# Performance work log

Measured on AMD Instinct MI355X. Metric: run time of the kernel, lower is better.

The kernel has to match this reference:

```python
import jax, jax.numpy as jnp
import numpy as np

NEG_SLOPE = 0.2


def _gat_layer(x, W, a_src, a_dst, b, src, dst, n_nodes):
    # x: [N, D_in], W: [D_in, D_out], a_src/a_dst: [D_out], b: [D_out]
    h = x @ W                                        # [N, D]
    e_src = h @ a_src                                # [N]
    e_dst = h @ a_dst                                # [N]
    e = jax.nn.leaky_relu(e_src[src] + e_dst[dst], NEG_SLOPE)  # [E]
    # segment softmax over incoming edges of each dst node
    m = jax.ops.segment_max(e, dst, num_segments=n_nodes)      # [N]
    w = jnp.exp(e - m[dst])                                    # [E]
    z = jax.ops.segment_sum(w, dst, num_segments=n_nodes)      # [N]
    alpha = w / z[dst]                                         # [E]
    out = jax.ops.segment_sum(h[src] * alpha[:, None], dst, num_segments=n_nodes)
    return out + b


def setup_inputs() -> dict:
    key = jax.random.key(0)
    ks = jax.random.split(key, 10)
    N, E, D = 10000, 100000, 768
    scale = 1.0 / np.sqrt(D)
    x = jax.random.normal(ks[0], (N, D), dtype=jnp.float32)
    edge_index = jax.random.randint(ks[1], (2, E), 0, N, dtype=jnp.int32)
    params = {}
    for i, nm in enumerate(["1", "2"]):
        params[f"W{nm}"] = jax.random.normal(ks[2 + 4 * i], (D, D), jnp.float32) * scale
        params[f"att_src{nm}"] = jax.random.normal(ks[3 + 4 * i], (D,), jnp.float32) * scale
        params[f"att_dst{nm}"] = jax.random.normal(ks[4 + 4 * i], (D,), jnp.float32) * scale
        params[f"b{nm}"] = jnp.zeros((D,), jnp.float32)
    return {"x": x, "edge_index": edge_index, **params}


def reference(x, edge_index, W1, att_src1, att_dst1, b1, W2, att_src2, att_dst2, b2):
    n_nodes = x.shape[0]
    loops = jnp.arange(n_nodes, dtype=edge_index.dtype)
    src = jnp.concatenate([edge_index[0], loops])  # add self loops (PyG default)
    dst = jnp.concatenate([edge_index[1], loops])
    h = _gat_layer(x, W1, att_src1, att_dst1, b1, src, dst, n_nodes)
    h = jax.nn.relu(h)
    out = _gat_layer(h, W2, att_src2, att_dst2, b2, src, dst, n_nodes)
    return out
```

## Files before the change

### kernel.cpp

```cpp
#include <hip/hip_runtime.h>
#include <hip/hip_bf16.h>

#define D_FEAT 768

typedef __bf16 bf16x8 __attribute__((ext_vector_type(8)));
typedef float floatx4 __attribute__((ext_vector_type(4)));

__device__ __forceinline__ float bf2f(unsigned short u) {
    unsigned int x = ((unsigned int)u) << 16;
    return __builtin_bit_cast(float, x);
}
__device__ __forceinline__ unsigned short f2bf(float f) {
    unsigned int x = __builtin_bit_cast(unsigned int, f);
    unsigned int lsb = (x >> 16) & 1u;
    x += 0x7fffu + lsb;
    return (unsigned short)(x >> 16);
}
__device__ __forceinline__ void async_ld16(const void* g, void* l) {
    __builtin_amdgcn_global_load_lds(
        (__attribute__((address_space(1))) void*)(g),
        (__attribute__((address_space(3))) void*)(l), 16, 0, 0);
}

__global__ __launch_bounds__(256) void conv_init_kernel(
    const float* __restrict__ x, unsigned short* __restrict__ xb, int n4,
    int* __restrict__ deg, float* __restrict__ es1, float* __restrict__ ed1,
    float* __restrict__ es2, float* __restrict__ ed2, int N)
{
    int i = blockIdx.x * 256 + threadIdx.x;
    if (i < n4) {
        float4 v = ((const float4*)x)[i];
        ushort4 o;
        o.x = f2bf(v.x); o.y = f2bf(v.y); o.z = f2bf(v.z); o.w = f2bf(v.w);
        ((ushort4*)xb)[i] = o;
    }
    if (i < N) {
        deg[i] = 1;
        es1[i] = 0.f; ed1[i] = 0.f; es2[i] = 0.f; ed2[i] = 0.f;
    }
}

__global__ __launch_bounds__(256) void transpose_kernel(
    const float* __restrict__ W1, const float* __restrict__ W2,
    unsigned short* __restrict__ Wt1, unsigned short* __restrict__ Wt2)
{
    const float* W = blockIdx.z ? W2 : W1;
    unsigned short* Wt = blockIdx.z ? Wt2 : Wt1;
    __shared__ float tile[32][33];
    int x0 = blockIdx.x * 32, y0 = blockIdx.y * 32;
    int tx = threadIdx.x & 31, ty = threadIdx.x >> 5;
    for (int r = ty; r < 32; r += 8)
        tile[r][tx] = W[(size_t)(y0 + r) * D_FEAT + x0 + tx];
    __syncthreads();
    for (int r = ty; r < 32; r += 8)
        Wt[(size_t)(x0 + r) * D_FEAT + y0 + tx] = f2bf(tile[tx][r]);
}

__global__ __launch_bounds__(256) void gemm_kernel(
    const unsigned short* __restrict__ A,
    const unsigned short* __restrict__ Bt,
    unsigned short* __restrict__ C,
    const float* __restrict__ vsrc, const float* __restrict__ vdst,
    float* __restrict__ es, float* __restrict__ ed, int M)
{
    __shared__ __align__(16) unsigned short sA[128 * 32];
    __shared__ __align__(16) unsigned short sB[128 * 32];

    const int tid = threadIdx.x;
    const int lane = tid & 63, wave = tid >> 6;
    const int m0 = blockIdx.x * 128, n0 = blockIdx.y * 128;
    const int wm = wave >> 1, wn = wave & 1;
    const int l15 = lane & 15, quad = lane >> 4;

    const int srow = lane >> 2;
    const int scol = (lane & 3) * 8;
    int ar0 = m0 + wave * 32 + srow;      if (ar0 >= M) ar0 = M - 1;
    int ar1 = m0 + wave * 32 + 16 + srow; if (ar1 >= M) ar1 = M - 1;
    const unsigned short* aptr0 = A + (size_t)ar0 * 768 + scol;
    const unsigned short* aptr1 = A + (size_t)ar1 * 768 + scol;
    const unsigned short* bptr0 = Bt + (size_t)(n0 + wave * 32 + srow) * 768 + scol;
    const unsigned short* bptr1 = bptr0 + (size_t)16 * 768;
    char* aldst = (char*)sA + wave * 2048;
    char* bldst = (char*)sB + wave * 2048;

    floatx4 acc[4][4];
    #pragma unroll
    for (int i = 0; i < 4; ++i)
        #pragma unroll
        for (int j = 0; j < 4; ++j)
            acc[i][j] = (floatx4){0.f, 0.f, 0.f, 0.f};

    for (int kt = 0; kt < 768; kt += 32) {
        __syncthreads();
        async_ld16(aptr0 + kt, aldst);
        async_ld16(aptr1 + kt, aldst + 1024);
        async_ld16(bptr0 + kt, bldst);
        async_ld16(bptr1 + kt, bldst + 1024);
        __syncthreads();

        bf16x8 af[4], bfr[4];
        #pragma unroll
        for (int i = 0; i < 4; ++i)
            af[i] = *(const bf16x8*)&sA[(wm * 64 + i * 16 + l15) * 32 + quad * 8];
        #pragma unroll
        for (int j = 0; j < 4; ++j)
            bfr[j] = *(const bf16x8*)&sB[(wn * 64 + j * 16 + l15) * 32 + quad * 8];
        #pragma unroll
        for (int i = 0; i < 4; ++i)
            #pragma unroll
            for (int j = 0; j < 4; ++j)
                acc[i][j] = __builtin_amdgcn_mfma_f32_16x16x32_bf16(af[i], bfr[j], acc[i][j], 0, 0, 0);
    }

    float as_[4], ad_[4];
    #pragma unroll
    for (int j = 0; j < 4; ++j) {
        int nn = n0 + wn * 64 + j * 16 + l15;
        as_[j] = vsrc[nn]; ad_[j] = vdst[nn];
    }

    #pragma unroll
    for (int i = 0; i < 4; ++i)
        #pragma unroll
        for (int r = 0; r < 4; ++r) {
            int m = m0 + wm * 64 + i * 16 + quad * 4 + r;
            float ps = 0.f, pd = 0.f;
            #pragma unroll
            for (int j = 0; j < 4; ++j) {
                float v = acc[i][j][r];
                ps += v * as_[j]; pd += v * ad_[j];
            }
            if (m < M) {
                #pragma unroll
                for (int j = 0; j < 4; ++j)
                    C[(size_t)m * 768 + n0 + wn * 64 + j * 16 + l15] = f2bf(acc[i][j][r]);
            }
            #pragma unroll
            for (int sh = 8; sh >= 1; sh >>= 1) {
                ps += __shfl_xor(ps, sh, 64);
                pd += __shfl_xor(pd, sh, 64);
            }
            if (l15 == 0 && m < M) {
                atomicAdd(&es[m], ps);
                atomicAdd(&ed[m], pd);
            }
        }
}

__global__ void count_kernel(const int* __restrict__ dst, int* __restrict__ deg, int e) {
    int i = blockIdx.x * blockDim.x + threadIdx.x;
    if (i < e) atomicAdd(&deg[dst[i]], 1);
}
__global__ __launch_bounds__(1024) void scan_kernel(
    const int* __restrict__ deg, int* __restrict__ row_ptr,
    int* __restrict__ cursor, int n)
{
    __shared__ int part[1024];
    int t = threadIdx.x;
    int per = (n + 1023) / 1024;
    int base = t * per;
    int s = 0;
    for (int i = 0; i < per; ++i) { int idx = base + i; if (idx < n) s += deg[idx]; }
    part[t] = s; __syncthreads();
    for (int off = 1; off < 1024; off <<= 1) {
        int v = (t >= off) ? part[t - off] : 0;
        __syncthreads();
        part[t] += v;
        __syncthreads();
    }
    int run = (t == 0) ? 0 : part[t - 1];
    for (int i = 0; i < per; ++i) {
        int idx = base + i;
        if (idx < n) { row_ptr[idx] = run; cursor[idx] = run; run += deg[idx]; }
    }
    if (t == 1023) row_ptr[n] = part[1023];
}
__global__ void fill_kernel(const int* __restrict__ src, const int* __restrict__ dst,
                            int* __restrict__ cursor, int* __restrict__ col_src,
                            int e, int n)
{
    int i = blockIdx.x * blockDim.x + threadIdx.x;
    if (i >= e + n) return;
    int s, d;
    if (i < e) { s = src[i]; d = dst[i]; } else { s = i - e; d = s; }
    int pos = atomicAdd(&cursor[d], 1);
    col_src[pos] = s;
}

__global__ __launch_bounds__(256) void agg_kernel(
    const unsigned short* __restrict__ h, const float* __restrict__ es,
    const float* __restrict__ ed, const int* __restrict__ row_ptr,
    const int* __restrict__ col_src, const float* __restrict__ bias,
    unsigned short* __restrict__ out_bf, float* __restrict__ out_f, int N)
{
    int wid = threadIdx.x >> 6, lane = threadIdx.x & 63;
    int n = blockIdx.x * 4 + wid;
    if (n >= N) return;
    int beg = row_ptr[n], end = row_ptr[n + 1], deg = end - beg;
    float edn = ed[n];

    float a[12];
    #pragma unroll
    for (int k = 0; k < 12; ++k) a[k] = 0.f;
    const unsigned short* hb = h + lane * 12;

    if (deg <= 64) {
        int s = 0; float v = -3.4e38f;
        if (lane < deg) {
            s = col_src[beg + lane];
            v = es[s] + edn;
            v = v > 0.f ? v : 0.2f * v;
        }
        float lm = v;
        #pragma unroll
        for (int m = 32; m >= 1; m >>= 1) lm = fmaxf(lm, __shfl_xor(lm, m, 64));
        float w = (lane < deg) ? __expf(v - lm) : 0.f;
        float ls = w;
        #pragma unroll
        for (int m = 32; m >= 1; m >>= 1) ls += __shfl_xor(ls, m, 64);
        w *= (1.f / ls);

        int i = 0;
        for (; i + 2 <= deg; i += 2) {
            int   s0 = __shfl(s, i, 64),     s1 = __shfl(s, i + 1, 64);
            float w0 = __shfl(w, i, 64),     w1 = __shfl(w, i + 1, 64);
            const unsigned short* h0 = hb + (size_t)s0 * 768;
            const unsigned short* h1 = hb + (size_t)s1 * 768;
            ushort4 p0 = *(const ushort4*)(h0);
            ushort4 p1 = *(const ushort4*)(h0 + 4);
            ushort4 p2 = *(const ushort4*)(h0 + 8);
            ushort4 q0 = *(const ushort4*)(h1);
            ushort4 q1 = *(const ushort4*)(h1 + 4);
            ushort4 q2 = *(const ushort4*)(h1 + 8);
            a[0]  += w0 * bf2f(p0.x) + w1 * bf2f(q0.x);
            a[1]  += w0 * bf2f(p0.y) + w1 * bf2f(q0.y);
            a[2]  += w0 * bf2f(p0.z) + w1 * bf2f(q0.z);
            a[3]  += w0 * bf2f(p0.w) + w1 * bf2f(q0.w);
            a[4]  += w0 * bf2f(p1.x) + w1 * bf2f(q1.x);
            a[5]  += w0 * bf2f(p1.y) + w1 * bf2f(q1.y);
            a[6]  += w0 * bf2f(p1.z) + w1 * bf2f(q1.z);
            a[7]  += w0 * bf2f(p1.w) + w1 * bf2f(q1.w);
            a[8]  += w0 * bf2f(p2.x) + w1 * bf2f(q2.x);
            a[9]  += w0 * bf2f(p2.y) + w1 * bf2f(q2.y);
            a[10] += w0 * bf2f(p2.z) + w1 * bf2f(q2.z);
            a[11] += w0 * bf2f(p2.w) + w1 * bf2f(q2.w);
        }
        if (i < deg) {
            int   s0 = __shfl(s, i, 64);
            float w0 = __shfl(w, i, 64);
            const unsigned short* h0 = hb + (size_t)s0 * 768;
            ushort4 p0 = *(const ushort4*)(h0);
            ushort4 p1 = *(const ushort4*)(h0 + 4);
            ushort4 p2 = *(const ushort4*)(h0 + 8);
            a[0]  += w0 * bf2f(p0.x); a[1]  += w0 * bf2f(p0.y);
            a[2]  += w0 * bf2f(p0.z); a[3]  += w0 * bf2f(p0.w);
            a[4]  += w0 * bf2f(p1.x); a[5]  += w0 * bf2f(p1.y);
            a[6]  += w0 * bf2f(p1.z); a[7]  += w0 * bf2f(p1.w);
            a[8]  += w0 * bf2f(p2.x); a[9]  += w0 * bf2f(p2.y);
            a[10] += w0 * bf2f(p2.z); a[11] += w0 * bf2f(p2.w);
        }
    } else {
        float lm = -3.4e38f;
        for (int i = beg + lane; i < end; i += 64) {
            float v = es[col_src[i]] + edn;
            v = v > 0.f ? v : 0.2f * v;
            lm = fmaxf(lm, v);
        }
        #pragma unroll
        for (int m = 32; m >= 1; m >>= 1) lm = fmaxf(lm, __shfl_xor(lm, m, 64));
        float ls = 0.f;
        for (int i = beg + lane; i < end; i += 64) {
            float v = es[col_src[i]] + edn;
            v = v > 0.f ? v : 0.2f * v;
            ls += __expf(v - lm);
        }
        #pragma unroll
        for (int m = 32; m >= 1; m >>= 1) ls += __shfl_xor(ls, m, 64);
        float rz = 1.f / ls;
        for (int i = beg; i < end; ++i) {
            int sidx = col_src[i];
            float u = es[sidx] + edn;
            u = u > 0.f ? u : 0.2f * u;
            float w = __expf(u - lm) * rz;
            const unsigned short* hr = hb + (size_t)sidx * 768;
            ushort4 v0 = *(const ushort4*)(hr);
            ushort4 v1 = *(const ushort4*)(hr + 4);
            ushort4 v2 = *(const ushort4*)(hr + 8);
            a[0]  += w * bf2f(v0.x); a[1]  += w * bf2f(v0.y);
            a[2]  += w * bf2f(v0.z); a[3]  += w * bf2f(v0.w);
            a[4]  += w * bf2f(v1.x); a[5]  += w * bf2f(v1.y);
            a[6]  += w * bf2f(v1.z); a[7]  += w * bf2f(v1.w);
            a[8]  += w * bf2f(v2.x); a[9]  += w * bf2f(v2.y);
            a[10] += w * bf2f(v2.z); a[11] += w * bf2f(v2.w);
        }
    }

    float4 bv0 = *(const float4*)&bias[lane * 12];
    float4 bv1 = *(const float4*)&bias[lane * 12 + 4];
    float4 bv2 = *(const float4*)&bias[lane * 12 + 8];
    float o[12];
    o[0] = a[0] + bv0.x; o[1] = a[1] + bv0.y; o[2] = a[2] + bv0.z; o[3] = a[3] + bv0.w;
    o[4] = a[4] + bv1.x; o[5] = a[5] + bv1.y; o[6] = a[6] + bv1.z; o[7] = a[7] + bv1.w;
    o[8] = a[8] + bv2.x; o[9] = a[9] + bv2.y; o[10] = a[10] + bv2.z; o[11] = a[11] + bv2.w;
    size_t base = (size_t)n * 768 + lane * 12;
    if (out_bf) {
        ushort4 w0, w1, w2;
        w0.x = f2bf(fmaxf(o[0], 0.f)); w0.y = f2bf(fmaxf(o[1], 0.f));
        w0.z = f2bf(fmaxf(o[2], 0.f)); w0.w = f2bf(fmaxf(o[3], 0.f));
        w1.x = f2bf(fmaxf(o[4], 0.f)); w1.y = f2bf(fmaxf(o[5], 0.f));
        w1.z = f2bf(fmaxf(o[6], 0.f)); w1.w = f2bf(fmaxf(o[7], 0.f));
        w2.x = f2bf(fmaxf(o[8], 0.f)); w2.y = f2bf(fmaxf(o[9], 0.f));
        w2.z = f2bf(fmaxf(o[10], 0.f)); w2.w = f2bf(fmaxf(o[11], 0.f));
        *(ushort4*)&out_bf[base] = w0;
        *(ushort4*)&out_bf[base + 4] = w1;
        *(ushort4*)&out_bf[base + 8] = w2;
    } else {
        float4 f0 = {o[0], o[1], o[2], o[3]};
        float4 f1 = {o[4], o[5], o[6], o[7]};
        float4 f2 = {o[8], o[9], o[10], o[11]};
        *(float4*)&out_f[base] = f0;
        *(float4*)&out_f[base + 4] = f1;
        *(float4*)&out_f[base + 8] = f2;
    }
}

extern "C" void kernel_launch(void* const* d_in, const int* in_sizes, int n_in,
                              void* d_out, int out_size, void* d_ws, size_t ws_size,
                              hipStream_t stream)
{
    const float* x   = (const float*)d_in[0];
    const int*   ei  = (const int*)d_in[1];
    const float* W1  = (const float*)d_in[2];
    const float* as1 = (const float*)d_in[3];
    const float* ad1 = (const float*)d_in[4];
    const float* b1  = (const float*)d_in[5];
    const float* W2  = (const float*)d_in[6];
    const float* as2 = (const float*)d_in[7];
    const float* ad2 = (const float*)d_in[8];
    const float* b2  = (const float*)d_in[9];

    const int N = in_sizes[0] / D_FEAT;
    const int E = in_sizes[1] / 2;
    const int* src = ei;
    const int* dst = ei + E;

    char* ws = (char*)d_ws;
    size_t off = 0;
    auto alloc = [&](size_t bytes) -> void* {
        void* p = ws + off;
        off += (bytes + 255) & ~(size_t)255;
        return p;
    };
    unsigned short* Wt1  = (unsigned short*)alloc((size_t)768 * 768 * 2);
    unsigned short* Wt2  = (unsigned short*)alloc((size_t)768 * 768 * 2);
    unsigned short* xb   = (unsigned short*)alloc((size_t)N * 768 * 2);
    unsigned short* h    = (unsigned short*)alloc((size_t)N * 768 * 2);
    unsigned short* x2b  = (unsigned short*)alloc((size_t)N * 768 * 2);
    float*          es1  = (float*)alloc((size_t)N * 4);
    float*          ed1  = (float*)alloc((size_t)N * 4);
    float*          es2  = (float*)alloc((size_t)N * 4);
    float*          ed2  = (float*)alloc((size_t)N * 4);
    int*            deg  = (int*)alloc((size_t)N * 4);
    int*            cur  = (int*)alloc((size_t)N * 4);
    int*            rowp = (int*)alloc((size_t)(N + 1) * 4);
    int*            col  = (int*)alloc((size_t)(E + N) * 4);

    int n4 = N * 768 / 4;
    conv_init_kernel<<<(n4 + 255) / 256, 256, 0, stream>>>(x, xb, n4, deg, es1, ed1, es2, ed2, N);
    dim3 tgrid(D_FEAT / 32, D_FEAT / 32, 2);
    transpose_kernel<<<tgrid, 256, 0, stream>>>(W1, W2, Wt1, Wt2);
    count_kernel<<<(E + 255) / 256, 256, 0, stream>>>(dst, deg, E);
    scan_kernel<<<1, 1024, 0, stream>>>(deg, rowp, cur, N);
    fill_kernel<<<(E + N + 255) / 256, 256, 0, stream>>>(src, dst, cur, col, E, N);

    dim3 ggrid((N + 127) / 128, D_FEAT / 128);
    gemm_kernel<<<ggrid, 256, 0, stream>>>(xb, Wt1, h, as1, ad1, es1, ed1, N);
    agg_kernel<<<(N + 3) / 4, 256, 0, stream>>>(h, es1, ed1, rowp, col, b1, x2b, nullptr, N);
    gemm_kernel<<<ggrid, 256, 0, stream>>>(x2b, Wt2, h, as2, ad2, es2, ed2, N);
    agg_kernel<<<(N + 3) / 4, 256, 0, stream>>>(h, es2, ed2, rowp, col, b2, nullptr, (float*)d_out, N);
}
```

Before: 238.1 us.

## Precompute W·a attention vectors and drop atomic score epilogue from GEMM

The attention scores e_src/e_dst are now computed as x·(W·a) rather than (x·W)·a. The projected vectors W·a are built in a merged prep kernel along with the transpose and the conversion. Layer-1 scores come from a per-node dot in the count kernel, and layer-2 scores are fused into the layer-1 aggregation epilogue. This removes the shuffle-reduce and global atomicAdd work from the GEMM epilogue and cuts the launch count. The aggregation gather loop is also unrolled by four. Scores now use bf16 x against fp32 W·a, so rounding differs slightly from the previous bf16 h path.

After: 231.0 us. 1.03x faster.

```diff
diff --git a/kernel.cpp b/kernel.cpp
--- a/kernel.cpp
+++ b/kernel.cpp
@@ -22,46 +22,109 @@
         (__attribute__((address_space(3))) void*)(l), 16, 0, 0);
 }
 
-__global__ __launch_bounds__(256) void conv_init_kernel(
-    const float* __restrict__ x, unsigned short* __restrict__ xb, int n4,
-    int* __restrict__ deg, float* __restrict__ es1, float* __restrict__ ed1,
-    float* __restrict__ es2, float* __restrict__ ed2, int N)
-{
-    int i = blockIdx.x * 256 + threadIdx.x;
-    if (i < n4) {
-        float4 v = ((const float4*)x)[i];
-        ushort4 o;
-        o.x = f2bf(v.x); o.y = f2bf(v.y); o.z = f2bf(v.z); o.w = f2bf(v.w);
-        ((ushort4*)xb)[i] = o;
-    }
-    if (i < N) {
-        deg[i] = 1;
-        es1[i] = 0.f; ed1[i] = 0.f; es2[i] = 0.f; ed2[i] = 0.f;
-    }
-}
-
-__global__ __launch_bounds__(256) void transpose_kernel(
+__global__ __launch_bounds__(256) void prep_kernel(
+    const float* __restrict__ x, unsigned short* __restrict__ xb, int n8,
     const float* __restrict__ W1, const float* __restrict__ W2,
-    unsigned short* __restrict__ Wt1, unsigned short* __restrict__ Wt2)
-{
-    const float* W = blockIdx.z ? W2 : W1;
-    unsigned short* Wt = blockIdx.z ? Wt2 : Wt1;
-    __shared__ float tile[32][33];
-    int x0 = blockIdx.x * 32, y0 = blockIdx.y * 32;
-    int tx = threadIdx.x & 31, ty = threadIdx.x >> 5;
-    for (int r = ty; r < 32; r += 8)
-        tile[r][tx] = W[(size_t)(y0 + r) * D_FEAT + x0 + tx];
-    __syncthreads();
-    for (int r = ty; r < 32; r += 8)
-        Wt[(size_t)(x0 + r) * D_FEAT + y0 + tx] = f2bf(tile[tx][r]);
+    unsigned short* __restrict__ Wt1, unsigned short* __restrict__ Wt2,
+    const float* __restrict__ as1, const float* __restrict__ ad1,
+    const float* __restrict__ as2, const float* __restrict__ ad2,
+    float* __restrict__ us1, float* __restrict__ ud1,
+    float* __restrict__ us2, float* __restrict__ ud2,
+    int* __restrict__ deg, int N)
+{
+    int b = blockIdx.x, tid = threadIdx.x;
+    if (b < 1152) {
+        const float* W = (b >= 576) ? W2 : W1;
+        unsigned short* Wt = (b >= 576) ? Wt2 : Wt1;
+        int rem = (b >= 576) ? b - 576 : b;
+        __shared__ float tile[32][33];
+        int x0 = (rem % 24) * 32, y0 = (rem / 24) * 32;
+        int tx = tid & 31, ty = tid >> 5;
+        for (int r = ty; r < 32; r += 8)
+            tile[r][tx] = W[(size_t)(y0 + r) * D_FEAT + x0 + tx];
+        __syncthreads();
+        for (int r = ty; r < 32; r += 8)
+            Wt[(size_t)(x0 + r) * D_FEAT + y0 + tx] = f2bf(tile[tx][r]);
+    } else if (b < 1344) {
+        int lane = tid & 63;
+        int k = (b - 1152) * 4 + (tid >> 6);
+        const float* r1 = W1 + (size_t)k * D_FEAT + lane * 12;
+        const float* r2 = W2 + (size_t)k * D_FEAT + lane * 12;
+        float s1 = 0.f, d1 = 0.f, s2 = 0.f, d2 = 0.f;
+        #pragma unroll
+        for (int c = 0; c < 3; ++c) {
+            float4 w1v = *(const float4*)(r1 + c * 4);
+            float4 w2v = *(const float4*)(r2 + c * 4);
+            int off = lane * 12 + c * 4;
+            float4 a1 = *(const float4*)(as1 + off);
+            float4 b1v = *(const float4*)(ad1 + off);
+            float4 a2 = *(const float4*)(as2 + off);
+            float4 b2v = *(const float4*)(ad2 + off);
+            s1 += w1v.x * a1.x + w1v.y * a1.y + w1v.z * a1.z + w1v.w * a1.w;
+            d1 += w1v.x * b1v.x + w1v.y * b1v.y + w1v.z * b1v.z + w1v.w * b1v.w;
+            s2 += w2v.x * a2.x + w2v.y * a2.y + w2v.z * a2.z + w2v.w * a2.w;
+            d2 += w2v.x * b2v.x + w2v.y * b2v.y + w2v.z * b2v.z + w2v.w * b2v.w;
+        }
+        #pragma unroll
+        for (int m = 32; m >= 1; m >>= 1) {
+            s1 += __shfl_xor(s1, m, 64); d1 += __shfl_xor(d1, m, 64);
+            s2 += __shfl_xor(s2, m, 64); d2 += __shfl_xor(d2, m, 64);
+        }
+        if (lane == 0) { us1[k] = s1; ud1[k] = d1; us2[k] = s2; ud2[k] = d2; }
+    } else {
+        int li = (b - 1344) * 256 + tid;
+        if (li < n8) {
+            float4 v0 = ((const float4*)x)[li * 2];
+            float4 v1 = ((const float4*)x)[li * 2 + 1];
+            ushort4 o0, o1;
+            o0.x = f2bf(v0.x); o0.y = f2bf(v0.y); o0.z = f2bf(v0.z); o0.w = f2bf(v0.w);
+            o1.x = f2bf(v1.x); o1.y = f2bf(v1.y); o1.z = f2bf(v1.z); o1.w = f2bf(v1.w);
+            ((ushort4*)xb)[li * 2] = o0;
+            ((ushort4*)xb)[li * 2 + 1] = o1;
+        }
+        if (li < N) deg[li] = 1;
+    }
+}
+
+__global__ __launch_bounds__(256) void count_dots_kernel(
+    const int* __restrict__ dst, int* __restrict__ deg, int E, int cB,
+    const unsigned short* __restrict__ xb,
+    const float* __restrict__ us1, const float* __restrict__ ud1,
+    float* __restrict__ es1, float* __restrict__ ed1, int N)
+{
+    int b = blockIdx.x, tid = threadIdx.x;
+    if (b < cB) {
+        int i = b * 256 + tid;
+        if (i < E) atomicAdd(&deg[dst[i]], 1);
+    } else {
+        int lane = tid & 63;
+        int n = (b - cB) * 4 + (tid >> 6);
+        if (n >= N) return;
+        const unsigned short* xr = xb + (size_t)n * D_FEAT + lane * 12;
+        float s = 0.f, d = 0.f;
+        #pragma unroll
+        for (int c = 0; c < 3; ++c) {
+            ushort4 v = *(const ushort4*)(xr + c * 4);
+            int off = lane * 12 + c * 4;
+            float4 u = *(const float4*)(us1 + off);
+            float4 w = *(const float4*)(ud1 + off);
+            float f0 = bf2f(v.x), f1 = bf2f(v.y), f2v = bf2f(v.z), f3 = bf2f(v.w);
+            s += f0 * u.x + f1 * u.y + f2v * u.z + f3 * u.w;
+            d += f0 * w.x + f1 * w.y + f2v * w.z + f3 * w.w;
+        }
+        #pragma unroll
+        for (int m = 32; m >= 1; m >>= 1) {
+            s += __shfl_xor(s, m, 64); d += __shfl_xor(d, m, 64);
+        }
+        if (lane == 0) { es1[n] = s; ed1[n] = d; }
+    }
 }
 
 __global__ __launch_bounds__(256) void gemm_kernel(
     const unsigned short* __restrict__ A,
     const unsigned short* __restrict__ Bt,
     unsigned short* __restrict__ C,
-    const float* __restrict__ vsrc, const float* __restrict__ vdst,
-    float* __restrict__ es, float* __restrict__ ed, int M)
+    int M)
 {
     __shared__ __align__(16) unsigned short sA[128 * 32];
     __shared__ __align__(16) unsigned short sB[128 * 32];
@@ -112,45 +175,19 @@
                 acc[i][j] = __builtin_amdgcn_mfma_f32_16x16x32_bf16(af[i], bfr[j], acc[i][j], 0, 0, 0);
     }
 
-    float as_[4], ad_[4];
-    #pragma unroll
-    for (int j = 0; j < 4; ++j) {
-        int nn = n0 + wn * 64 + j * 16 + l15;
-        as_[j] = vsrc[nn]; ad_[j] = vdst[nn];
-    }
-
     #pragma unroll
     for (int i = 0; i < 4; ++i)
         #pragma unroll
         for (int r = 0; r < 4; ++r) {
             int m = m0 + wm * 64 + i * 16 + quad * 4 + r;
-            float ps = 0.f, pd = 0.f;
-            #pragma unroll
-            for (int j = 0; j < 4; ++j) {
-                float v = acc[i][j][r];
-                ps += v * as_[j]; pd += v * ad_[j];
-            }
             if (m < M) {
                 #pragma unroll
                 for (int j = 0; j < 4; ++j)
                     C[(size_t)m * 768 + n0 + wn * 64 + j * 16 + l15] = f2bf(acc[i][j][r]);
             }
-            #pragma unroll
-            for (int sh = 8; sh >= 1; sh >>= 1) {
-                ps += __shfl_xor(ps, sh, 64);
-                pd += __shfl_xor(pd, sh, 64);
-            }
-            if (l15 == 0 && m < M) {
-                atomicAdd(&es[m], ps);
-                atomicAdd(&ed[m], pd);
-            }
-        }
-}
-
-__global__ void count_kernel(const int* __restrict__ dst, int* __restrict__ deg, int e) {
-    int i = blockIdx.x * blockDim.x + threadIdx.x;
-    if (i < e) atomicAdd(&deg[dst[i]], 1);
-}
+        }
+}
+
 __global__ __launch_bounds__(1024) void scan_kernel(
     const int* __restrict__ deg, int* __restrict__ row_ptr,
     int* __restrict__ cursor, int n)
@@ -191,7 +228,9 @@
     const unsigned short* __restrict__ h, const float* __restrict__ es,
     const float* __restrict__ ed, const int* __restrict__ row_ptr,
     const int* __restrict__ col_src, const float* __restrict__ bias,
-    unsigned short* __restrict__ out_bf, float* __restrict__ out_f, int N)
+    unsigned short* __restrict__ out_bf, float* __restrict__ out_f,
+    const float* __restrict__ us2, const float* __restrict__ ud2,
+    float* __restrict__ es2, float* __restrict__ ed2, int N)
 {
     int wid = threadIdx.x >> 6, lane = threadIdx.x & 63;
     int n = blockIdx.x * 4 + wid;
@@ -221,31 +260,24 @@
         w *= (1.f / ls);
 
         int i = 0;
-        for (; i + 2 <= deg; i += 2) {
-            int   s0 = __shfl(s, i, 64),     s1 = __shfl(s, i + 1, 64);
-            float w0 = __shfl(w, i, 64),     w1 = __shfl(w, i + 1, 64);
-            const unsigned short* h0 = hb + (size_t)s0 * 768;
-            const unsigned short* h1 = hb + (size_t)s1 * 768;
-            ushort4 p0 = *(const ushort4*)(h0);
-            ushort4 p1 = *(const ushort4*)(h0 + 4);
-            ushort4 p2 = *(const ushort4*)(h0 + 8);
-            ushort4 q0 = *(const ushort4*)(h1);
-            ushort4 q1 = *(const ushort4*)(h1 + 4);
-            ushort4 q2 = *(const ushort4*)(h1 + 8);
-            a[0]  += w0 * bf2f(p0.x) + w1 * bf2f(q0.x);
-            a[1]  += w0 * bf2f(p0.y) + w1 * bf2f(q0.y);
-            a[2]  += w0 * bf2f(p0.z) + w1 * bf2f(q0.z);
-            a[3]  += w0 * bf2f(p0.w) + w1 * bf2f(q0.w);
-            a[4]  += w0 * bf2f(p1.x) + w1 * bf2f(q1.x);
-            a[5]  += w0 * bf2f(p1.y) + w1 * bf2f(q1.y);
-            a[6]  += w0 * bf2f(p1.z) + w1 * bf2f(q1.z);
-            a[7]  += w0 * bf2f(p1.w) + w1 * bf2f(q1.w);
-            a[8]  += w0 * bf2f(p2.x) + w1 * bf2f(q2.x);
-            a[9]  += w0 * bf2f(p2.y) + w1 * bf2f(q2.y);
-            a[10] += w0 * bf2f(p2.z) + w1 * bf2f(q2.z);
-            a[11] += w0 * bf2f(p2.w) + w1 * bf2f(q2.w);
-        }
-        if (i < deg) {
+        for (; i + 4 <= deg; i += 4) {
+            #pragma unroll
+            for (int u = 0; u < 4; ++u) {
+                int   su = __shfl(s, i + u, 64);
+                float wu = __shfl(w, i + u, 64);
+                const unsigned short* hr = hb + (size_t)su * 768;
+                ushort4 p0 = *(const ushort4*)(hr);
+                ushort4 p1 = *(const ushort4*)(hr + 4);
+                ushort4 p2 = *(const ushort4*)(hr + 8);
+                a[0]  += wu * bf2f(p0.x); a[1]  += wu * bf2f(p0.y);
+                a[2]  += wu * bf2f(p0.z); a[3]  += wu * bf2f(p0.w);
+                a[4]  += wu * bf2f(p1.x); a[5]  += wu * bf2f(p1.y);
+                a[6]  += wu * bf2f(p1.z); a[7]  += wu * bf2f(p1.w);
+                a[8]  += wu * bf2f(p2.x); a[9]  += wu * bf2f(p2.y);
+                a[10] += wu * bf2f(p2.z); a[11] += wu * bf2f(p2.w);
+            }
+        }
+        for (; i < deg; ++i) {
             int   s0 = __shfl(s, i, 64);
             float w0 = __shfl(w, i, 64);
             const unsigned short* h0 = hb + (size_t)s0 * 768;
@@ -304,13 +336,26 @@
     o[8] = a[8] + bv2.x; o[9] = a[9] + bv2.y; o[10] = a[10] + bv2.z; o[11] = a[11] + bv2.w;
     size_t base = (size_t)n * 768 + lane * 12;
     if (out_bf) {
+        #pragma unroll
+        for (int k = 0; k < 12; ++k) o[k] = fmaxf(o[k], 0.f);
+        float ps = 0.f, pd = 0.f;
+        #pragma unroll
+        for (int c = 0; c < 3; ++c) {
+            int off = lane * 12 + c * 4;
+            float4 u = *(const float4*)(us2 + off);
+            float4 w = *(const float4*)(ud2 + off);
+            ps += o[c*4] * u.x + o[c*4+1] * u.y + o[c*4+2] * u.z + o[c*4+3] * u.w;
+            pd += o[c*4] * w.x + o[c*4+1] * w.y + o[c*4+2] * w.z + o[c*4+3] * w.w;
+        }
+        #pragma unroll
+        for (int m = 32; m >= 1; m >>= 1) {
+            ps += __shfl_xor(ps, m, 64); pd += __shfl_xor(pd, m, 64);
+        }
+        if (lane == 0) { es2[n] = ps; ed2[n] = pd; }
         ushort4 w0, w1, w2;
-        w0.x = f2bf(fmaxf(o[0], 0.f)); w0.y = f2bf(fmaxf(o[1], 0.f));
-        w0.z = f2bf(fmaxf(o[2], 0.f)); w0.w = f2bf(fmaxf(o[3], 0.f));
-        w1.x = f2bf(fmaxf(o[4], 0.f)); w1.y = f2bf(fmaxf(o[5], 0.f));
-        w1.z = f2bf(fmaxf(o[6], 0.f)); w1.w = f2bf(fmaxf(o[7], 0.f));
-        w2.x = f2bf(fmaxf(o[8], 0.f)); w2.y = f2bf(fmaxf(o[9], 0.f));
-        w2.z = f2bf(fmaxf(o[10], 0.f)); w2.w = f2bf(fmaxf(o[11], 0.f));
+        w0.x = f2bf(o[0]); w0.y = f2bf(o[1]); w0.z = f2bf(o[2]); w0.w = f2bf(o[3]);
+        w1.x = f2bf(o[4]); w1.y = f2bf(o[5]); w1.z = f2bf(o[6]); w1.w = f2bf(o[7]);
+        w2.x = f2bf(o[8]); w2.y = f2bf(o[9]); w2.z = f2bf(o[10]); w2.w = f2bf(o[11]);
         *(ushort4*)&out_bf[base] = w0;
         *(ushort4*)&out_bf[base + 4] = w1;
         *(ushort4*)&out_bf[base + 8] = w2;
@@ -356,6 +401,10 @@
     unsigned short* xb   = (unsigned short*)alloc((size_t)N * 768 * 2);
     unsigned short* h    = (unsigned short*)alloc((size_t)N * 768 * 2);
     unsigned short* x2b  = (unsigned short*)alloc((size_t)N * 768 * 2);
+    float*          us1  = (float*)alloc((size_t)768 * 4);
+    float*          ud1  = (float*)alloc((size_t)768 * 4);
+    float*          us2  = (float*)alloc((size_t)768 * 4);
+    float*          ud2  = (float*)alloc((size_t)768 * 4);
     float*          es1  = (float*)alloc((size_t)N * 4);
     float*          ed1  = (float*)alloc((size_t)N * 4);
     float*          es2  = (float*)alloc((size_t)N * 4);
@@ -365,17 +414,23 @@
     int*            rowp = (int*)alloc((size_t)(N + 1) * 4);
     int*            col  = (int*)alloc((size_t)(E + N) * 4);
 
-    int n4 = N * 768 / 4;
-    conv_init_kernel<<<(n4 + 255) / 256, 256, 0, stream>>>(x, xb, n4, deg, es1, ed1, es2, ed2, N);
-    dim3 tgrid(D_FEAT / 32, D_FEAT / 32, 2);
-    transpose_kernel<<<tgrid, 256, 0, stream>>>(W1, W2, Wt1, Wt2);
-    count_kernel<<<(E + 255) / 256, 256, 0, stream>>>(dst, deg, E);
+    int n8 = N * 768 / 8;
+    int convBlocks = (n8 + 255) / 256;
+    prep_kernel<<<1344 + convBlocks, 256, 0, stream>>>(
+        x, xb, n8, W1, W2, Wt1, Wt2, as1, ad1, as2, ad2,
+        us1, ud1, us2, ud2, deg, N);
+    int cB = (E + 255) / 256;
+    count_dots_kernel<<<cB + (N + 3) / 4, 256, 0, stream>>>(
+        dst, deg, E, cB, xb, us1, ud1, es1, ed1, N);
     scan_kernel<<<1, 1024, 0, stream>>>(deg, rowp, cur, N);
     fill_kernel<<<(E + N + 255) / 256, 256, 0, stream>>>(src, dst, cur, col, E, N);
 
     dim3 ggrid((N + 127) / 128, D_FEAT / 128);
-    gemm_kernel<<<ggrid, 256, 0, stream>>>(xb, Wt1, h, as1, ad1, es1, ed1, N);
-    agg_kernel<<<(N + 3) / 4, 256, 0, stream>>>(h, es1, ed1, rowp, col, b1, x2b, nullptr, N);
-    gemm_kernel<<<ggrid, 256, 0, stream>>>(x2b, Wt2, h, as2, ad2, es2, ed2, N);
-    agg_kernel<<<(N + 3) / 4, 256, 0, stream>>>(h, es2, ed2, rowp, col, b2, nullptr, (float*)d_out, N);
-}
+    gemm_kernel<<<ggrid, 256, 0, stream>>>(xb, Wt1, h, N);
+    agg_kernel<<<(N + 3) / 4, 256, 0, stream>>>(h, es1, ed1, rowp, col, b1,
+                                                x2b, nullptr, us2, ud2, es2, ed2, N);
+    gemm_kernel<<<ggrid, 256, 0, stream>>>(x2b, Wt2, h, N);
+    agg_kernel<<<(N + 3) / 4, 256, 0, stream>>>(h, es2, ed2, rowp, col, b2,
+                                                nullptr, (float*)d_out,
+                                                nullptr, nullptr, nullptr, nullptr, N);
+}
```
